# Performance work log

Hardware: AMD Instinct MI355X
Metric: run time of the kernel (lower is better)

The kernel has to match this reference:

```python
import jax, jax.numpy as jnp
import numpy as np

B, N, C, H = 4, 2048, 768, 12
D = C // H  # head_dim = 64

def setup_inputs() -> dict:
    key = jax.random.key(0)
    ks = jax.random.split(key, 6)
    s = 0.02
    return {
        "img_tokens": jax.random.normal(ks[0], (B, N, C), jnp.float32),
        "ln_gamma": jnp.ones((C,), jnp.float32),
        "ln_beta": jnp.zeros((C,), jnp.float32),
        "w_qkv": jax.random.normal(ks[1], (C, 3 * C), jnp.float32) * s,
        "w_out": jax.random.normal(ks[2], (C, C), jnp.float32) * s,
        "b_out": jnp.zeros((C,), jnp.float32),
    }

def reference(img_tokens, ln_gamma, ln_beta, w_qkv, w_out, b_out):
    x = img_tokens
    # LayerNorm over channel dim
    mu = jnp.mean(x, axis=-1, keepdims=True)
    var = jnp.var(x, axis=-1, keepdims=True)
    xn = (x - mu) * jax.lax.rsqrt(var + 1e-5) * ln_gamma + ln_beta
    qkv = xn @ w_qkv                      # [B, N, 3C]
    q, k, v = jnp.split(qkv, 3, axis=-1)
    def heads(t):                          # [B, N, C] -> [B, H, N, D]
        return t.reshape(B, N, H, D).transpose(0, 2, 1, 3)
    q, k, v = heads(q), heads(k), heads(v)
    scale = 1.0 / np.sqrt(D).astype(np.float32)
    scores = jnp.einsum('bhnd,bhmd->bhnm', q, k) * scale  # [B, H, N, N]
    attn = jax.nn.softmax(scores, axis=-1)
    out = jnp.einsum('bhnm,bhmd->bhnd', attn, v)          # [B, H, N, D]
    out = out.transpose(0, 2, 1, 3).reshape(B, N, C)
    out = out @ w_out + b_out
    return out + img_tokens
```

## Files before the change

### kernel.cpp

```cpp
#include <hip/hip_runtime.h>


typedef __bf16 bf16x8 __attribute__((ext_vector_type(8)));
typedef float  f32x4  __attribute__((ext_vector_type(4)));
typedef unsigned int u32x4 __attribute__((ext_vector_type(4)));

#define MFMA16(a,b,c) __builtin_amdgcn_mfma_f32_16x16x32_bf16((a),(b),(c),0,0,0)

__device__ inline f32x4 zero4() { f32x4 z = {0.f,0.f,0.f,0.f}; return z; }

__device__ inline void gll16(const __bf16* g, __bf16* l) {
  __builtin_amdgcn_global_load_lds((const __attribute__((address_space(1))) unsigned int*)g,
                                   (__attribute__((address_space(3))) unsigned int*)l,
                                   16, 0, 0);
}

__device__ inline unsigned cvt_pk_bf16(float lo, float hi) {
  unsigned r;
  asm("v_cvt_pk_bf16_f32 %0, %1, %2" : "=v"(r) : "v"(lo), "v"(hi));
  return r;
}
__device__ inline void permlane32_swap(unsigned &a, unsigned &b) {
  asm("v_permlane32_swap_b32 %0, %1" : "+v"(a), "+v"(b));
}
__device__ inline void permlane16_swap(unsigned &a, unsigned &b) {
  asm("v_permlane16_swap_b32 %0, %1" : "+v"(a), "+v"(b));
}

__global__ __launch_bounds__(256) void ln_kernel(const float* __restrict__ x,
                                                 const float* __restrict__ g,
                                                 const float* __restrict__ bt,
                                                 __bf16* __restrict__ xn) {
  const int row = blockIdx.x;
  const int tid = threadIdx.x;
  const float* xr = x + (size_t)row * 768;
  float v[3]; float s = 0.f, ss = 0.f;
  #pragma unroll
  for (int i = 0; i < 3; ++i) { float f = xr[tid + 256*i]; v[i] = f; s += f; ss += f*f; }
  #pragma unroll
  for (int m = 32; m >= 1; m >>= 1) { s += __shfl_xor(s, m, 64); ss += __shfl_xor(ss, m, 64); }
  __shared__ float red[8];
  const int wave = tid >> 6;
  if ((tid & 63) == 0) { red[wave] = s; red[4 + wave] = ss; }
  __syncthreads();
  s  = red[0] + red[1] + red[2] + red[3];
  ss = red[4] + red[5] + red[6] + red[7];
  const float mu  = s * (1.f/768.f);
  const float var = ss * (1.f/768.f) - mu*mu;
  const float inv = rsqrtf(var + 1e-5f);
  __bf16* xo = xn + (size_t)row * 768;
  #pragma unroll
  for (int i = 0; i < 3; ++i) {
    const int c0 = tid + 256*i;
    xo[c0] = (__bf16)((v[i] - mu) * inv * g[c0] + bt[c0]);
  }
}

__global__ __launch_bounds__(256) void transpose_kernel(const float* __restrict__ in,
                                                        __bf16* __restrict__ out,
                                                        int R, int C) {
  __shared__ float t[32][33];
  const int tx = threadIdx.x & 31, ty = threadIdx.x >> 5;
  const int c0 = blockIdx.x * 32, r0 = blockIdx.y * 32;
  #pragma unroll
  for (int p = 0; p < 4; ++p) t[ty + 8*p][tx] = in[(size_t)(r0 + ty + 8*p) * C + c0 + tx];
  __syncthreads();
  #pragma unroll
  for (int p = 0; p < 4; ++p) out[(size_t)(c0 + ty + 8*p) * R + r0 + tx] = (__bf16)t[tx][ty + 8*p];
}

template<int KDIM>
__device__ inline void gemm_mainloop(const __bf16* __restrict__ A, const __bf16* __restrict__ BT,
                                     int bm, int bn, int wave, int lane,
                                     f32x4 acc[4][4], __bf16* Asm, __bf16* Bsm) {
  const int wm = wave >> 1, wn = wave & 1;
  const int lr = lane & 15, lk = lane >> 4;
  constexpr int NIT = KDIM / 64;
  auto stage = [&](int t) {
    const int k0 = t * 64;
    __bf16* Ad = Asm + (t & 1) * 8192;
    __bf16* Bd = Bsm + (t & 1) * 8192;
    #pragma unroll
    for (int s2 = 0; s2 < 4; ++s2) {
      const int st = wave * 4 + s2;
      const int rb = st >> 1, kh = st & 1;
      gll16(A  + (size_t)(bm + rb*16 + lr) * KDIM + k0 + kh*32 + lk*8, Ad + st*512);
      gll16(BT + (size_t)(bn + rb*16 + lr) * KDIM + k0 + kh*32 + lk*8, Bd + st*512);
    }
  };
  stage(0);
  stage(1);
  for (int t = 0; t < NIT; ++t) {
    if (t + 1 < NIT) asm volatile("s_waitcnt vmcnt(8)" ::: "memory");
    else             asm volatile("s_waitcnt vmcnt(0)" ::: "memory");
    asm volatile("s_barrier" ::: "memory");
    const __bf16* Ab = Asm + (t & 1) * 8192;
    const __bf16* Bb = Bsm + (t & 1) * 8192;
    #pragma unroll
    for (int ks = 0; ks < 2; ++ks) {
      bf16x8 a[4], b[4];
      #pragma unroll
      for (int mt = 0; mt < 4; ++mt) a[mt] = *(const bf16x8*)(Ab + ((wm*4+mt)*2+ks)*512 + lane*8);
      #pragma unroll
      for (int nt = 0; nt < 4; ++nt) b[nt] = *(const bf16x8*)(Bb + ((wn*4+nt)*2+ks)*512 + lane*8);
      __builtin_amdgcn_s_setprio(1);
      #pragma unroll
      for (int mt = 0; mt < 4; ++mt)
        #pragma unroll
        for (int nt = 0; nt < 4; ++nt)
          acc[mt][nt] = MFMA16(a[mt], b[nt], acc[mt][nt]);
      __builtin_amdgcn_s_setprio(0);
    }
    asm volatile("s_barrier" ::: "memory");
    if (t + 2 < NIT) stage(t + 2);
  }
}

__global__ __launch_bounds__(256) void gemm_qkv_kernel(const __bf16* __restrict__ A,
                                                       const __bf16* __restrict__ BT,
                                                       __bf16* __restrict__ q,
                                                       __bf16* __restrict__ k,
                                                       __bf16* __restrict__ vt) {
  __shared__ __align__(16) __bf16 smem[4*8192];
  __bf16* Asm = smem;
  __bf16* Bsm = smem + 2*8192;
  const int lane = threadIdx.x & 63, wave = threadIdx.x >> 6;
  const int wg = (blockIdx.x & 7) * 144 + (blockIdx.x >> 3);
  const int bm = (wg / 18) * 128, bn = (wg % 18) * 128;
  f32x4 acc[4][4];
  #pragma unroll
  for (int i = 0; i < 4; ++i)
    #pragma unroll
    for (int j = 0; j < 4; ++j) acc[i][j] = zero4();
  gemm_mainloop<768>(A, BT, bm, bn, wave, lane, acc, Asm, Bsm);
  const int wm = wave >> 1, wn = wave & 1;
  const int quad = lane >> 4, c = lane & 15;
  if (bn < 1536) {
    const float qscale = 0.125f * 1.44269504088896f;
    #pragma unroll
    for (int mt = 0; mt < 4; ++mt)
      #pragma unroll
      for (int nt = 0; nt < 4; ++nt) {
        const int col = bn + wn*64 + nt*16 + c;
        const int which = col >= 768 ? 1 : 0;
        const int within = col - which*768;
        const int h = within >> 6, d = within & 63;
        #pragma unroll
        for (int r = 0; r < 4; ++r) {
          const int row = bm + wm*64 + mt*16 + quad*4 + r;
          const int b = row >> 11, n = row & 2047;
          const float vv = acc[mt][nt][r];
          const size_t idx = ((size_t)(b*12 + h) * 2048 + n) * 64 + d;
          if (which == 0) q[idx] = (__bf16)(vv * qscale);
          else            k[idx] = (__bf16)vv;
        }
      }
  } else {
    __syncthreads();
    #pragma unroll
    for (int mt = 0; mt < 4; ++mt)
      #pragma unroll
      for (int nt = 0; nt < 4; ++nt) {
        const int lcol = wn*64 + nt*16 + c;
        #pragma unroll
        for (int r = 0; r < 4; ++r) {
          const int lrow = wm*64 + mt*16 + quad*4 + r;
          smem[lrow*66 + lcol] = (__bf16)acc[mt][nt][r];
        }
      }
    __syncthreads();
    const int b = bm >> 11, n0 = bm & 2047;
    const int vo = bn - 1536;
    const int n = threadIdx.x & 127;
    const int csel = threadIdx.x >> 7;
    #pragma unroll
    for (int pass = 0; pass < 64; ++pass) {
      const int lc = pass*2 + csel;
      const int gcol = vo + lc;
      const int h = gcol >> 6, d = gcol & 63;
      vt[((size_t)(b*12 + h)*64 + d)*2048 + n0 + n] = smem[n*66 + lc];
    }
  }
}

__global__ __launch_bounds__(256) void gemm_out_kernel(const __bf16* __restrict__ A,
                                                       const __bf16* __restrict__ BT,
                                                       const float* __restrict__ bias,
                                                       const float* __restrict__ resid,
                                                       float* __restrict__ out) {
  __shared__ __align__(16) __bf16 Asm[2*8192];
  __shared__ __align__(16) __bf16 Bsm[2*8192];
  const int lane = threadIdx.x & 63, wave = threadIdx.x >> 6;
  const int wg = (blockIdx.x & 7) * 48 + (blockIdx.x >> 3);
  const int bm = (wg / 6) * 128, bn = (wg % 6) * 128;
  f32x4 acc[4][4];
  #pragma unroll
  for (int i = 0; i < 4; ++i)
    #pragma unroll
    for (int j = 0; j < 4; ++j) acc[i][j] = zero4();
  gemm_mainloop<768>(A, BT, bm, bn, wave, lane, acc, Asm, Bsm);
  const int wm = wave >> 1, wn = wave & 1;
  const int quad = lane >> 4, c = lane & 15;
  #pragma unroll
  for (int mt = 0; mt < 4; ++mt)
    #pragma unroll
    for (int nt = 0; nt < 4; ++nt) {
      const int col = bn + wn*64 + nt*16 + c;
      #pragma unroll
      for (int r = 0; r < 4; ++r) {
        const int row = bm + wm*64 + mt*16 + quad*4 + r;
        out[(size_t)row*768 + col] = acc[mt][nt][r] + bias[col] + resid[(size_t)row*768 + col];
      }
    }
}

__global__ __launch_bounds__(512, 6) void attn_kernel(const __bf16* __restrict__ q,
                                                      const __bf16* __restrict__ k,
                                                      const __bf16* __restrict__ vt,
                                                      __bf16* __restrict__ o) {
  const int xcd = blockIdx.x & 7, i = blockIdx.x >> 3;
  const int bh = xcd * 6 + (i >> 4);
  const int qt = i & 15;
  const int lane = threadIdx.x & 63, wave = threadIdx.x >> 6;
  const int c = lane & 15, quad = lane >> 4;
  const int lr = lane & 15, lk = lane >> 4;
  const int q0 = qt*128 + wave*16;

  const __bf16* qb = q  + ((size_t)bh*2048 + q0) * 64;
  const __bf16* kb = k  + (size_t)bh * 2048 * 64;
  const __bf16* vb = vt + (size_t)bh * 64 * 2048;

  __shared__ __align__(16) __bf16 Ksm[2][4096];
  __shared__ __align__(16) __bf16 Vsm[2][4096];

  bf16x8 aq[2];
  aq[0] = *(const bf16x8*)(qb + (size_t)c*64 + quad*8);
  aq[1] = *(const bf16x8*)(qb + (size_t)c*64 + 32 + quad*8);

  const __bf16 one = (__bf16)1.0f;
  bf16x8 vones;
  #pragma unroll
  for (int j = 0; j < 8; ++j) vones[j] = one;

  f32x4 od[4];
  f32x4 clacc = zero4();
  #pragma unroll
  for (int r = 0; r < 4; ++r) od[r] = zero4();

  auto stage = [&](int it) {
    const int kt = it * 64;
    __bf16* Ks = Ksm[it & 1];
    __bf16* Vs = Vsm[it & 1];
    gll16(kb + (size_t)(kt + (wave>>1)*16 + lr) * 64 + (wave&1)*32 + lk*8,  Ks + wave*512);
    gll16(vb + (size_t)((wave>>1)*16 + lr) * 2048 + kt + (wave&1)*32 + lk*8, Vs + wave*512);
  };

  stage(0);
  stage(1);

  for (int it = 0; it < 32; ++it) {
    const __bf16* Ks = Ksm[it & 1];
    const __bf16* Vs = Vsm[it & 1];
    if (it < 31) asm volatile("s_waitcnt vmcnt(2)" ::: "memory");
    else         asm volatile("s_waitcnt vmcnt(0)" ::: "memory");
    asm volatile("s_barrier" ::: "memory");
    #pragma unroll
    for (int ch = 0; ch < 2; ++ch) {
      unsigned pk[2][2];
      #pragma unroll
      for (int t2 = 0; t2 < 2; ++t2) {
        const int t = ch*2 + t2;
        const bf16x8 ka0 = *(const bf16x8*)(Ks + (t*2+0)*512 + lane*8);
        const bf16x8 ka1 = *(const bf16x8*)(Ks + (t*2+1)*512 + lane*8);
        f32x4 z = zero4();
        __builtin_amdgcn_s_setprio(1);
        z = MFMA16(ka0, aq[0], z);
        z = MFMA16(ka1, aq[1], z);
        __builtin_amdgcn_s_setprio(0);
        const float p0 = __builtin_amdgcn_exp2f(z[0]);
        const float p1 = __builtin_amdgcn_exp2f(z[1]);
        const float p2 = __builtin_amdgcn_exp2f(z[2]);
        const float p3 = __builtin_amdgcn_exp2f(z[3]);
        pk[t2][0] = cvt_pk_bf16(p0, p1);
        pk[t2][1] = cvt_pk_bf16(p2, p3);
      }
      unsigned s0 = pk[0][0], s2 = pk[1][0];
      permlane32_swap(s0, s2);
      permlane16_swap(s0, s2);
      unsigned s1 = pk[0][1], s3 = pk[1][1];
      permlane32_swap(s1, s3);
      permlane16_swap(s1, s3);
      u32x4 w4; w4.x = s0; w4.y = s1; w4.z = s2; w4.w = s3;
      const bf16x8 pa = __builtin_bit_cast(bf16x8, w4);
      __builtin_amdgcn_s_setprio(1);
      #pragma unroll
      for (int dt = 0; dt < 4; ++dt) {
        const bf16x8 bv = *(const bf16x8*)(Vs + (dt*2+ch)*512 + lane*8);
        od[dt] = MFMA16(pa, bv, od[dt]);
      }
      clacc = MFMA16(pa, vones, clacc);
      __builtin_amdgcn_s_setprio(0);
    }
    asm volatile("s_barrier" ::: "memory");
    if (it + 2 < 32) stage(it + 2);
  }
  const int b = bh / 12, h = bh % 12;
  float rl[4];
  #pragma unroll
  for (int r = 0; r < 4; ++r) rl[r] = 1.f / clacc[r];
  #pragma unroll
  for (int dt = 0; dt < 4; ++dt)
    #pragma unroll
    for (int r = 0; r < 4; ++r) {
      const int n = q0 + quad*4 + r;
      const int col = h*64 + dt*16 + c;
      o[((size_t)b*2048 + n)*768 + col] = (__bf16)(od[dt][r] * rl[r]);
    }
}

extern "C" void kernel_launch(void* const* d_in, const int* in_sizes, int n_in,
                              void* d_out, int out_size, void* d_ws, size_t ws_size,
                              hipStream_t stream) {
  const float* img   = (const float*)d_in[0];
  const float* gamma = (const float*)d_in[1];
  const float* beta  = (const float*)d_in[2];
  const float* wqkv  = (const float*)d_in[3];
  const float* wout  = (const float*)d_in[4];
  const float* bout  = (const float*)d_in[5];
  float* out = (float*)d_out;

  __bf16* ws = (__bf16*)d_ws;
  size_t off = 0;
  __bf16* xn    = ws + off; off += (size_t)8192*768;
  __bf16* wqkvT = ws + off; off += (size_t)2304*768;
  __bf16* woutT = ws + off; off += (size_t)768*768;
  __bf16* qs    = ws + off; off += (size_t)48*2048*64;
  __bf16* ks    = ws + off; off += (size_t)48*2048*64;
  __bf16* vts   = ws + off; off += (size_t)48*64*2048;
  __bf16* os    = ws + off; off += (size_t)8192*768;

  ln_kernel<<<8192, 256, 0, stream>>>(img, gamma, beta, xn);
  transpose_kernel<<<dim3(72, 24), 256, 0, stream>>>(wqkv, wqkvT, 768, 2304);
  transpose_kernel<<<dim3(24, 24), 256, 0, stream>>>(wout, woutT, 768, 768);
  gemm_qkv_kernel<<<1152, 256, 0, stream>>>(xn, wqkvT, qs, ks, vts);
  attn_kernel<<<768, 512, 0, stream>>>(qs, ks, vts, os);
  gemm_out_kernel<<<384, 256, 0, stream>>>(os, woutT, bout, img, out);
}
```

Measured before the change: 239.4 us.

## Load K tiles directly into registers instead of staging through LDS

```diff
diff --git a/kernel.cpp b/kernel.cpp
--- a/kernel.cpp
+++ b/kernel.cpp
@@ -230,7 +230,6 @@
   const __bf16* kb = k  + (size_t)bh * 2048 * 64;
   const __bf16* vb = vt + (size_t)bh * 64 * 2048;
 
-  __shared__ __align__(16) __bf16 Ksm[2][4096];
   __shared__ __align__(16) __bf16 Vsm[2][4096];
 
   bf16x8 aq[2];
@@ -247,22 +246,26 @@
   #pragma unroll
   for (int r = 0; r < 4; ++r) od[r] = zero4();
 
-  auto stage = [&](int it) {
+  bf16x8 kr[8];
+  #pragma unroll
+  for (int st = 0; st < 8; ++st)
+    kr[st] = *(const bf16x8*)(kb + (size_t)((st>>1)*16 + lr) * 64 + (st&1)*32 + lk*8);
+
+  auto stageV = [&](int it) {
     const int kt = it * 64;
-    __bf16* Ks = Ksm[it & 1];
-    __bf16* Vs = Vsm[it & 1];
-    gll16(kb + (size_t)(kt + (wave>>1)*16 + lr) * 64 + (wave&1)*32 + lk*8,  Ks + wave*512);
-    gll16(vb + (size_t)((wave>>1)*16 + lr) * 2048 + kt + (wave&1)*32 + lk*8, Vs + wave*512);
+    gll16(vb + (size_t)((wave>>1)*16 + lr) * 2048 + kt + (wave&1)*32 + lk*8,
+          Vsm[it & 1] + wave*512);
   };
 
-  stage(0);
-  stage(1);
+  stageV(0);
+  stageV(1);
 
   for (int it = 0; it < 32; ++it) {
-    const __bf16* Ks = Ksm[it & 1];
     const __bf16* Vs = Vsm[it & 1];
-    if (it < 31) asm volatile("s_waitcnt vmcnt(2)" ::: "memory");
-    else         asm volatile("s_waitcnt vmcnt(0)" ::: "memory");
+    const int ktn = (it + 1) * 64;
+    if (it == 0)      asm volatile("s_waitcnt vmcnt(1)" ::: "memory");
+    else if (it < 31) asm volatile("s_waitcnt vmcnt(9)" ::: "memory");
+    else              asm volatile("s_waitcnt vmcnt(8)" ::: "memory");
     asm volatile("s_barrier" ::: "memory");
     #pragma unroll
     for (int ch = 0; ch < 2; ++ch) {
@@ -270,12 +273,10 @@
       #pragma unroll
       for (int t2 = 0; t2 < 2; ++t2) {
         const int t = ch*2 + t2;
-        const bf16x8 ka0 = *(const bf16x8*)(Ks + (t*2+0)*512 + lane*8);
-        const bf16x8 ka1 = *(const bf16x8*)(Ks + (t*2+1)*512 + lane*8);
         f32x4 z = zero4();
         __builtin_amdgcn_s_setprio(1);
-        z = MFMA16(ka0, aq[0], z);
-        z = MFMA16(ka1, aq[1], z);
+        z = MFMA16(kr[t*2+0], aq[0], z);
+        z = MFMA16(kr[t*2+1], aq[1], z);
         __builtin_amdgcn_s_setprio(0);
         const float p0 = __builtin_amdgcn_exp2f(z[0]);
         const float p1 = __builtin_amdgcn_exp2f(z[1]);
@@ -283,6 +284,13 @@
         const float p3 = __builtin_amdgcn_exp2f(z[3]);
         pk[t2][0] = cvt_pk_bf16(p0, p1);
         pk[t2][1] = cvt_pk_bf16(p2, p3);
+      }
+      if (it < 31) {
+        #pragma unroll
+        for (int j = 0; j < 4; ++j) {
+          const int st = ch*4 + j;
+          kr[st] = *(const bf16x8*)(kb + (size_t)(ktn + (st>>1)*16 + lr) * 64 + (st&1)*32 + lk*8);
+        }
       }
       unsigned s0 = pk[0][0], s2 = pk[1][0];
       permlane32_swap(s0, s2);
@@ -302,7 +310,7 @@
       __builtin_amdgcn_s_setprio(0);
     }
     asm volatile("s_barrier" ::: "memory");
-    if (it + 2 < 32) stage(it + 2);
+    if (it + 2 < 32) stageV(it + 2);
   }
   const int b = bh / 12, h = bh % 12;
   float rl[4];
```

Measured after the change: 384.8 us. +60.7%, slower.

## Rewrite QKV GEMM with 256x256 tiles, 8 waves and quarter-staged pipelining

Applied to the files above, without the earlier changes.

```diff
diff --git a/kernel.cpp b/kernel.cpp
--- a/kernel.cpp
+++ b/kernel.cpp
@@ -116,69 +116,151 @@
   }
 }
 
-__global__ __launch_bounds__(256) void gemm_qkv_kernel(const __bf16* __restrict__ A,
-                                                       const __bf16* __restrict__ BT,
-                                                       __bf16* __restrict__ q,
-                                                       __bf16* __restrict__ k,
-                                                       __bf16* __restrict__ vt) {
-  __shared__ __align__(16) __bf16 smem[4*8192];
+__global__ __launch_bounds__(512, 2) void gemm_qkv_kernel(const __bf16* __restrict__ A,
+                                                          const __bf16* __restrict__ BT,
+                                                          __bf16* __restrict__ q,
+                                                          __bf16* __restrict__ k,
+                                                          __bf16* __restrict__ vt) {
+  __shared__ __align__(16) __bf16 smem[65536];
   __bf16* Asm = smem;
-  __bf16* Bsm = smem + 2*8192;
+  __bf16* Bsm = smem + 32768;
   const int lane = threadIdx.x & 63, wave = threadIdx.x >> 6;
-  const int wg = (blockIdx.x & 7) * 144 + (blockIdx.x >> 3);
-  const int bm = (wg / 18) * 128, bn = (wg % 18) * 128;
-  f32x4 acc[4][4];
-  #pragma unroll
-  for (int i = 0; i < 4; ++i)
+  const int wm = wave >> 2, wn = wave & 3;
+  const int lr = lane & 15, lk = lane >> 4;
+  const int quad = lane >> 4, c = lane & 15;
+  const int wg = ((int)blockIdx.x & 7) * 36 + ((int)blockIdx.x >> 3);
+  const int bm = (wg / 9) * 256, bn = (wg % 9) * 256;
+  constexpr int KD = 768;
+  constexpr int NT = 12;
+
+  auto AOFF = [](int buf, int half, int st) { return ((buf*2 + half)*16 + st)*512; };
+
+  auto stageA = [&](int T, int h) {
+    const int b = T & 1;
+    #pragma unroll
+    for (int kh = 0; kh < 2; ++kh)
+      gll16(A + (size_t)(bm + h*128 + wave*16 + lr) * KD + T*64 + kh*32 + lk*8,
+            Asm + AOFF(b, h, wave*2 + kh));
+  };
+  auto stageB = [&](int T, int h) {
+    const int b = T & 1;
+    #pragma unroll
+    for (int kh = 0; kh < 2; ++kh)
+      gll16(BT + (size_t)(bn + h*128 + wave*16 + lr) * KD + T*64 + kh*32 + lk*8,
+            Bsm + AOFF(b, h, wave*2 + kh));
+  };
+
+  f32x4 acc[8][4];
+  #pragma unroll
+  for (int i = 0; i < 8; ++i)
     #pragma unroll
     for (int j = 0; j < 4; ++j) acc[i][j] = zero4();
-  gemm_mainloop<768>(A, BT, bm, bn, wave, lane, acc, Asm, Bsm);
-  const int wm = wave >> 1, wn = wave & 1;
-  const int quad = lane >> 4, c = lane & 15;
+
+  stageA(0, 0); stageB(0, 0); stageA(0, 1); stageB(0, 1); stageA(1, 0); stageB(1, 0);
+  asm volatile("s_waitcnt vmcnt(4)" ::: "memory");
+  asm volatile("s_barrier" ::: "memory");
+
+  bf16x8 ac[4][2];
+  bf16x8 b0[2][2];
+  bf16x8 b1[2][2];
+
+  for (int T = 0; T < NT; ++T) {
+    const int buf = T & 1;
+    #pragma unroll
+    for (int qp = 0; qp < 4; ++qp) {
+      const int mh = qp >> 1, nh = qp & 1;
+      if (nh == 0) {
+        #pragma unroll
+        for (int mf = 0; mf < 4; ++mf)
+          #pragma unroll
+          for (int ks = 0; ks < 2; ++ks)
+            ac[mf][ks] = *(const bf16x8*)(Asm + AOFF(buf, mh, (wm*4+mf)*2+ks) + lane*8);
+      }
+      if (qp == 0) {
+        #pragma unroll
+        for (int nf = 0; nf < 2; ++nf)
+          #pragma unroll
+          for (int ks = 0; ks < 2; ++ks)
+            b0[nf][ks] = *(const bf16x8*)(Bsm + AOFF(buf, 0, (wn*2+nf)*2+ks) + lane*8);
+      } else if (qp == 1) {
+        #pragma unroll
+        for (int nf = 0; nf < 2; ++nf)
+          #pragma unroll
+          for (int ks = 0; ks < 2; ++ks)
+            b1[nf][ks] = *(const bf16x8*)(Bsm + AOFF(buf, 1, (wn*2+nf)*2+ks) + lane*8);
+      }
+      if (qp == 0) { if (T + 1 < NT) stageA(T + 1, 1); }
+      else if (qp == 1) { if (T + 1 < NT) stageB(T + 1, 1); }
+      else if (qp == 2) { if (T + 2 < NT) stageA(T + 2, 0); }
+      else {
+        if (T + 2 < NT) stageB(T + 2, 0);
+        if (T + 2 < NT)      asm volatile("s_waitcnt vmcnt(4)" ::: "memory");
+        else if (T + 1 < NT) asm volatile("s_waitcnt vmcnt(0)" ::: "memory");
+      }
+      asm volatile("s_barrier" ::: "memory");
+      __builtin_amdgcn_s_setprio(1);
+      #pragma unroll
+      for (int mf = 0; mf < 4; ++mf)
+        #pragma unroll
+        for (int nf = 0; nf < 2; ++nf)
+          #pragma unroll
+          for (int ks = 0; ks < 2; ++ks) {
+            const bf16x8 bb = (nh == 0) ? b0[nf][ks] : b1[nf][ks];
+            acc[mh*4+mf][nh*2+nf] = MFMA16(ac[mf][ks], bb, acc[mh*4+mf][nh*2+nf]);
+          }
+      __builtin_amdgcn_s_setprio(0);
+      asm volatile("s_barrier" ::: "memory");
+    }
+  }
+
   if (bn < 1536) {
     const float qscale = 0.125f * 1.44269504088896f;
     #pragma unroll
-    for (int mt = 0; mt < 4; ++mt)
-      #pragma unroll
-      for (int nt = 0; nt < 4; ++nt) {
-        const int col = bn + wn*64 + nt*16 + c;
+    for (int mf = 0; mf < 8; ++mf)
+      #pragma unroll
+      for (int nf = 0; nf < 4; ++nf) {
+        const int col = bn + (nf>>1)*128 + wn*32 + (nf&1)*16 + c;
         const int which = col >= 768 ? 1 : 0;
         const int within = col - which*768;
         const int h = within >> 6, d = within & 63;
         #pragma unroll
         for (int r = 0; r < 4; ++r) {
-          const int row = bm + wm*64 + mt*16 + quad*4 + r;
+          const int row = bm + (mf>>2)*128 + wm*64 + (mf&3)*16 + quad*4 + r;
           const int b = row >> 11, n = row & 2047;
-          const float vv = acc[mt][nt][r];
+          const float vv = acc[mf][nf][r];
           const size_t idx = ((size_t)(b*12 + h) * 2048 + n) * 64 + d;
           if (which == 0) q[idx] = (__bf16)(vv * qscale);
           else            k[idx] = (__bf16)vv;
         }
       }
   } else {
-    __syncthreads();
-    #pragma unroll
-    for (int mt = 0; mt < 4; ++mt)
-      #pragma unroll
-      for (int nt = 0; nt < 4; ++nt) {
-        const int lcol = wn*64 + nt*16 + c;
-        #pragma unroll
-        for (int r = 0; r < 4; ++r) {
-          const int lrow = wm*64 + mt*16 + quad*4 + r;
-          smem[lrow*66 + lcol] = (__bf16)acc[mt][nt][r];
-        }
-      }
-    __syncthreads();
     const int b = bm >> 11, n0 = bm & 2047;
     const int vo = bn - 1536;
-    const int n = threadIdx.x & 127;
-    const int csel = threadIdx.x >> 7;
-    #pragma unroll
-    for (int pass = 0; pass < 64; ++pass) {
-      const int lc = pass*2 + csel;
-      const int gcol = vo + lc;
-      const int h = gcol >> 6, d = gcol & 63;
-      vt[((size_t)(b*12 + h)*64 + d)*2048 + n0 + n] = smem[n*66 + lc];
+    #pragma unroll
+    for (int ch2 = 0; ch2 < 2; ++ch2) {
+      __syncthreads();
+      #pragma unroll
+      for (int mf = 0; mf < 8; ++mf)
+        #pragma unroll
+        for (int nf2 = 0; nf2 < 2; ++nf2) {
+          const int nf = ch2*2 + nf2;
+          const int lcol = wn*32 + (nf&1)*16 + c;
+          #pragma unroll
+          for (int r = 0; r < 4; ++r) {
+            const int lrow = (mf>>2)*128 + wm*64 + (mf&3)*16 + quad*4 + r;
+            smem[lrow*130 + lcol] = (__bf16)acc[mf][nf][r];
+          }
+        }
+      __syncthreads();
+      const int n = threadIdx.x & 255;
+      const int csel = (threadIdx.x >> 8) & 1;
+      #pragma unroll
+      for (int pass = 0; pass < 64; ++pass) {
+        const int lc = pass*2 + csel;
+        const int gcol = vo + ch2*128 + lc;
+        const int h = gcol >> 6, d = gcol & 63;
+        vt[((size_t)(b*12 + h)*64 + d)*2048 + n0 + n] = smem[n*130 + lc];
+      }
     }
   }
 }
@@ -191,7 +273,7 @@
   __shared__ __align__(16) __bf16 Asm[2*8192];
   __shared__ __align__(16) __bf16 Bsm[2*8192];
   const int lane = threadIdx.x & 63, wave = threadIdx.x >> 6;
-  const int wg = (blockIdx.x & 7) * 48 + (blockIdx.x >> 3);
+  const int wg = ((int)blockIdx.x & 7) * 48 + ((int)blockIdx.x >> 3);
   const int bm = (wg / 6) * 128, bn = (wg % 6) * 128;
   f32x4 acc[4][4];
   #pragma unroll
@@ -342,7 +424,7 @@
   ln_kernel<<<8192, 256, 0, stream>>>(img, gamma, beta, xn);
   transpose_kernel<<<dim3(72, 24), 256, 0, stream>>>(wqkv, wqkvT, 768, 2304);
   transpose_kernel<<<dim3(24, 24), 256, 0, stream>>>(wout, woutT, 768, 768);
-  gemm_qkv_kernel<<<1152, 256, 0, stream>>>(xn, wqkvT, qs, ks, vts);
+  gemm_qkv_kernel<<<288, 512, 0, stream>>>(xn, wqkvT, qs, ks, vts);
   attn_kernel<<<768, 512, 0, stream>>>(qs, ks, vts, os);
   gemm_out_kernel<<<384, 256, 0, stream>>>(os, woutT, bout, img, out);
 }
```

Measured after the change: 243.9 us. Within noise of the previous version (+1.9%).
